# Kernel tuning notes

Hardware: AMD Instinct MI355X
Metric: run time of the kernel (lower is better)

The kernel has to match this reference:

```python
import jax, jax.numpy as jnp
import numpy as np

GRID_SIZE = 8
SPLINE_ORDER = 3
LAYERS = [256, 512, 512, 256]  # [input_dim] + hidden_dims
BATCH = 8192
BN_EPS = 1e-5


def make_grid(in_features):
    # efficient-kan/torchkan grid: uniform on [-1, 1] extended by spline_order on each side
    h = 2.0 / GRID_SIZE
    g = jnp.arange(-SPLINE_ORDER, GRID_SIZE + SPLINE_ORDER + 1, dtype=jnp.float32) * h - 1.0
    return jnp.broadcast_to(g, (in_features, g.shape[0]))  # (In, G + 2k + 1)


def b_splines(x, grid):
    # x: (B, In), grid: (In, G + 2k + 1) -> bases: (B, In, G + k)
    xg = x[:, :, None]
    bases = ((xg >= grid[:, :-1]) & (xg < grid[:, 1:])).astype(x.dtype)
    for k in range(1, SPLINE_ORDER + 1):
        left = (xg - grid[:, : -(k + 1)]) / (grid[:, k:-1] - grid[:, : -(k + 1)])
        right = (grid[:, k + 1 :] - xg) / (grid[:, k + 1 :] - grid[:, 1:-k])
        bases = left * bases[:, :, :-1] + right * bases[:, :, 1:]
    return bases


def kan_linear(x, grid, base_w, spline_w):
    # base path: GELU (exact, matching torch.nn.GELU) then linear
    base_out = jax.nn.gelu(x, approximate=False) @ base_w.T
    spline_out = jnp.einsum('bik,oik->bo', b_splines(x, grid), spline_w)
    return base_out + spline_out


def setup_inputs() -> dict:
    key = jax.random.key(0)
    ks = jax.random.split(key, 16)
    inp = {'x': jax.random.normal(ks[0], (BATCH, LAYERS[0]), dtype=jnp.float32)}
    n_bases = GRID_SIZE + SPLINE_ORDER
    for i, (fin, fout) in enumerate(zip(LAYERS[:-1], LAYERS[1:])):
        scale = 1.0 / np.sqrt(fin)
        inp[f'grid{i}'] = make_grid(fin)
        inp[f'base_w{i}'] = jax.random.normal(ks[1 + 3 * i], (fout, fin), dtype=jnp.float32) * scale
        inp[f'spline_w{i}'] = jax.random.normal(ks[2 + 3 * i], (fout, fin, n_bases), dtype=jnp.float32) * (0.1 * scale)
    d_out = LAYERS[-1]
    inp['bn_gamma'] = jnp.ones((d_out,), dtype=jnp.float32)
    inp['bn_beta'] = jnp.zeros((d_out,), dtype=jnp.float32)
    inp['bn_mean'] = jax.random.normal(ks[10], (d_out,), dtype=jnp.float32) * 0.1
    inp['bn_var'] = jax.random.uniform(ks[11], (d_out,), dtype=jnp.float32, minval=0.5, maxval=1.5)
    return inp


def reference(x, grid0, base_w0, spline_w0, grid1, base_w1, spline_w1, grid2, base_w2, spline_w2, bn_gamma, bn_beta, bn_mean, bn_var):
    h = kan_linear(x, grid0, base_w0, spline_w0)
    h = kan_linear(h, grid1, base_w1, spline_w1)
    h = kan_linear(h, grid2, base_w2, spline_w2)
    # BatchNorm1d in eval mode (running stats); Dropout is identity at inference
    return bn_gamma * (h - bn_mean) * jax.lax.rsqrt(bn_var + BN_EPS) + bn_beta
```

## Files before the change

kernel.cpp:

```cpp
#include <hip/hip_runtime.h>
#include <hip/hip_bf16.h>
#include <cstdint>


typedef unsigned short ushort_t;
typedef __bf16 bf16x8 __attribute__((ext_vector_type(8)));
typedef float f32x4 __attribute__((ext_vector_type(4)));

__device__ __forceinline__ ushort_t f2bf(float f) {
    __bf16 h = (__bf16)f;
    return __builtin_bit_cast(ushort_t, h);
}

__device__ __forceinline__ void gload_lds16(const void* g, void* lds) {
    __builtin_amdgcn_global_load_lds(
        (const __attribute__((address_space(1))) unsigned int*)(uintptr_t)g,
        (__attribute__((address_space(3))) unsigned int*)(unsigned int)(uintptr_t)lds,
        16, 0, 0);
}

__device__ __forceinline__ void expand12(float x, ushort_t* o) {
    float x3 = x * x * x;
    float y  = 0.7978845608028654f * (x + 0.044715f * x3);
    float e  = __expf(2.0f * y);
    float th = 1.0f - 2.0f / (e + 1.0f);
    o[0] = f2bf(0.5f * x * (1.0f + th));
    float xs = (x + 1.75f) * 4.0f;
#pragma unroll
    for (int j = 0; j < 11; ++j) {
        float t  = xs - (float)j;
        float a  = fabsf(t - 2.0f);
        float p1 = (3.0f * a - 6.0f) * a * a + 4.0f;
        float c  = 2.0f - a;
        float p2 = c * c * c;
        float v  = (a <= 1.0f) ? p1 : fmaxf(p2, 0.0f);
        o[1 + j] = f2bf(v * (1.0f / 6.0f));
    }
}

template <bool SUM>
__global__ __launch_bounds__(256) void expand_kernel(
    const float* __restrict__ X0, const float* __restrict__ X1,
    ushort_t* __restrict__ A, int total2)
{
    int idx = blockIdx.x * 256 + threadIdx.x;
    if (idx >= total2) return;
    float2 h = *(const float2*)(X0 + 2 * (size_t)idx);
    if (SUM) {
        float2 h2 = *(const float2*)(X1 + 2 * (size_t)idx);
        h.x += h2.x; h.y += h2.y;
    }
    union { ushort_t us[24]; uint4 v[3]; } pk;
    expand12(h.x, pk.us);
    expand12(h.y, pk.us + 12);
    uint4* dst = (uint4*)(A + (size_t)idx * 24);
    dst[0] = pk.v[0]; dst[1] = pk.v[1]; dst[2] = pk.v[2];
}

__global__ __launch_bounds__(256) void pack_w_kernel(
    const float* __restrict__ bw, const float* __restrict__ sw,
    ushort_t* __restrict__ W, int total)
{
    int idx = blockIdx.x * 256 + threadIdx.x;
    if (idx >= total) return;
    union { ushort_t us[12]; uint2 v[3]; } pk;
    pk.us[0] = f2bf(bw[idx]);
    const float* s = sw + (size_t)idx * 11;
#pragma unroll
    for (int k = 0; k < 11; ++k) pk.us[1 + k] = f2bf(s[k]);
    uint2* dst = (uint2*)(W + (size_t)idx * 12);
    dst[0] = pk.v[0]; dst[1] = pk.v[1]; dst[2] = pk.v[2];
}

__global__ __launch_bounds__(256, 2) void gemm_kernel(
    const ushort_t* __restrict__ A,
    const ushort_t* __restrict__ W,
    float* __restrict__ C,
    int M, int N, int K, int kcps)
{
    __shared__ __align__(16) ushort_t As[128 * 64];
    __shared__ __align__(16) ushort_t Bs[128 * 64];

    const int t   = threadIdx.x;
    const int l   = t & 63;
    const int w   = t >> 6;
    const int wm  = w >> 1;
    const int wn  = w & 1;
    const int l15 = l & 15;
    const int q   = l >> 4;
    const int blockM = blockIdx.x * 128;
    const int blockN = blockIdx.y * 128;
    const int kb0 = blockIdx.z * kcps, kb1 = kb0 + kcps;
    float* Cz = C + (size_t)blockIdx.z * M * N;

    f32x4 acc[4][4];
#pragma unroll
    for (int i = 0; i < 4; ++i)
#pragma unroll
        for (int j = 0; j < 4; ++j) acc[i][j] = (f32x4){0.f, 0.f, 0.f, 0.f};

    for (int kb = kb0; kb < kb1; ++kb) {
        const int k0 = kb << 6;
#pragma unroll
        for (int it = 0; it < 4; ++it) {
            int s   = it * 256 + t;
            int row = s >> 3, c = s & 7;
            int g   = c ^ (row & 7);
            gload_lds16(A + ((size_t)(blockM + row) * K + k0 + g * 8), &As[s * 8]);
        }
#pragma unroll
        for (int it = 0; it < 4; ++it) {
            int s   = it * 256 + t;
            int row = s >> 3, c = s & 7;
            int g   = c ^ (row & 7);
            gload_lds16(W + ((size_t)(blockN + row) * K + k0 + g * 8), &Bs[s * 8]);
        }
        __syncthreads();

#pragma unroll
        for (int ks = 0; ks < 2; ++ks) {
            const int kc = ks * 4 + q;
            bf16x8 af[4], bf[4];
#pragma unroll
            for (int mi = 0; mi < 4; ++mi) {
                int m  = wm * 64 + mi * 16 + l15;
                int cs = kc ^ (m & 7);
                af[mi] = *(const bf16x8*)&As[(size_t)(m * 8 + cs) * 8];
            }
#pragma unroll
            for (int ni = 0; ni < 4; ++ni) {
                int n  = wn * 64 + ni * 16 + l15;
                int cs = kc ^ (n & 7);
                bf[ni] = *(const bf16x8*)&Bs[(size_t)(n * 8 + cs) * 8];
            }
#pragma unroll
            for (int mi = 0; mi < 4; ++mi)
#pragma unroll
                for (int ni = 0; ni < 4; ++ni)
                    acc[mi][ni] = __builtin_amdgcn_mfma_f32_16x16x32_bf16(
                        af[mi], bf[ni], acc[mi][ni], 0, 0, 0);
        }
        __syncthreads();
    }

#pragma unroll
    for (int ni = 0; ni < 4; ++ni) {
        int n = blockN + wn * 64 + ni * 16 + l15;
#pragma unroll
        for (int mi = 0; mi < 4; ++mi) {
            int mb = blockM + wm * 64 + mi * 16 + q * 4;
#pragma unroll
            for (int r = 0; r < 4; ++r)
                Cz[(size_t)(mb + r) * N + n] = acc[mi][ni][r];
        }
    }
}

__global__ __launch_bounds__(256) void bn_reduce_kernel(
    const float4* __restrict__ Q0, const float4* __restrict__ Q1,
    const float4* __restrict__ Q2, const float4* __restrict__ Q3,
    const float* __restrict__ gamma, const float* __restrict__ beta,
    const float* __restrict__ mean,  const float* __restrict__ var,
    float4* __restrict__ out, int n4)
{
    int i = blockIdx.x * 256 + threadIdx.x;
    if (i >= n4) return;
    float4 a = Q0[i], b = Q1[i], c = Q2[i], d = Q3[i];
    int nb = (i * 4) & 255;
    float4 g  = *(const float4*)(gamma + nb);
    float4 be = *(const float4*)(beta + nb);
    float4 mn = *(const float4*)(mean + nb);
    float4 vr = *(const float4*)(var + nb);
    float4 o;
    o.x = g.x * rsqrtf(vr.x + 1e-5f) * (a.x + b.x + c.x + d.x - mn.x) + be.x;
    o.y = g.y * rsqrtf(vr.y + 1e-5f) * (a.y + b.y + c.y + d.y - mn.y) + be.y;
    o.z = g.z * rsqrtf(vr.z + 1e-5f) * (a.z + b.z + c.z + d.z - mn.z) + be.z;
    o.w = g.w * rsqrtf(vr.w + 1e-5f) * (a.w + b.w + c.w + d.w - mn.w) + be.w;
    out[i] = o;
}

extern "C" void kernel_launch(void* const* d_in, const int* in_sizes, int n_in,
                              void* d_out, int out_size, void* d_ws, size_t ws_size,
                              hipStream_t stream) {
    const float* x     = (const float*)d_in[0];
    const float* bw0   = (const float*)d_in[2];
    const float* sw0   = (const float*)d_in[3];
    const float* bw1   = (const float*)d_in[5];
    const float* sw1   = (const float*)d_in[6];
    const float* bw2   = (const float*)d_in[8];
    const float* sw2   = (const float*)d_in[9];
    const float* gamma = (const float*)d_in[10];
    const float* beta  = (const float*)d_in[11];
    const float* mean  = (const float*)d_in[12];
    const float* var   = (const float*)d_in[13];

    char* ws = (char*)d_ws;
    ushort_t* Abuf = (ushort_t*)(ws);
    ushort_t* W0   = (ushort_t*)(ws + 100663296);
    ushort_t* W1   = (ushort_t*)(ws + 103809024);
    ushort_t* W2   = (ushort_t*)(ws + 110100480);
    float*    P0   = (float*)(ws + 113246208);
    float*    P1   = (float*)(ws + 130023424);
    float*    Q0   = (float*)(ws + 113246208);
    float*    Q1   = (float*)(ws + 121634816);
    float*    Q2   = (float*)(ws + 130023424);
    float*    Q3   = (float*)(ws + 138412032);
    float*    out  = (float*)d_out;

    pack_w_kernel<<<(512 * 256 + 255) / 256, 256, 0, stream>>>(bw0, sw0, W0, 512 * 256);
    pack_w_kernel<<<(512 * 512 + 255) / 256, 256, 0, stream>>>(bw1, sw1, W1, 512 * 512);
    pack_w_kernel<<<(256 * 512 + 255) / 256, 256, 0, stream>>>(bw2, sw2, W2, 256 * 512);

    expand_kernel<false><<<4096, 256, 0, stream>>>(x, nullptr, Abuf, 8192 * 256 / 2);
    {
        dim3 g(64, 4, 2);
        gemm_kernel<<<g, 256, 0, stream>>>(Abuf, W0, P0, 8192, 512, 3072, 24);
    }
    expand_kernel<true><<<8192, 256, 0, stream>>>(P0, P1, Abuf, 8192 * 512 / 2);
    {
        dim3 g(64, 4, 2);
        gemm_kernel<<<g, 256, 0, stream>>>(Abuf, W1, P0, 8192, 512, 6144, 48);
    }
    expand_kernel<true><<<8192, 256, 0, stream>>>(P0, P1, Abuf, 8192 * 512 / 2);
    {
        dim3 g(64, 2, 4);
        gemm_kernel<<<g, 256, 0, stream>>>(Abuf, W2, Q0, 8192, 256, 6144, 24);
    }
    bn_reduce_kernel<<<2048, 256, 0, stream>>>(
        (const float4*)Q0, (const float4*)Q1, (const float4*)Q2, (const float4*)Q3,
        gamma, beta, mean, var, (float4*)out, 8192 * 256 / 4);
}
```

Baseline: 305.1 us.

## Rewrite GEMM as 128x256 tile with triple-buffered LDS prefetch pipeline

The GEMM now uses 512-thread blocks, each computing a 128x256 output tile with 8 waves (2x4). K-tiles are staged into three LDS slots held in dynamic shared memory, loading two tiles ahead. The loads are interleaved with four MFMA phases per tile, separated by barriers, raised scheduling priority (s_setprio) and explicit vmcnt and lgkmcnt waits. The aim is to hide global-to-LDS latency and improve operand reuse. The costs are 144 KB of LDS per block, which limits occupancy, many more barriers per tile, and a grid half as wide in N.

Measured after the change: 303.9 us. No clear change (-0.4%).

```diff
diff --git a/kernel.cpp b/kernel.cpp
--- a/kernel.cpp
+++ b/kernel.cpp
@@ -72,75 +72,172 @@
     dst[0] = pk.v[0]; dst[1] = pk.v[1]; dst[2] = pk.v[2];
 }
 
-__global__ __launch_bounds__(256, 2) void gemm_kernel(
+#define SLOT 24576
+#define ASZ  8192
+
+__global__ __launch_bounds__(512, 2) void gemm_kernel(
     const ushort_t* __restrict__ A,
     const ushort_t* __restrict__ W,
     float* __restrict__ C,
     int M, int N, int K, int kcps)
 {
-    __shared__ __align__(16) ushort_t As[128 * 64];
-    __shared__ __align__(16) ushort_t Bs[128 * 64];
+    extern __shared__ __align__(16) ushort_t lds[];
 
     const int t   = threadIdx.x;
     const int l   = t & 63;
     const int w   = t >> 6;
-    const int wm  = w >> 1;
-    const int wn  = w & 1;
+    const int wm  = w >> 2;
+    const int wn  = w & 3;
     const int l15 = l & 15;
     const int q   = l >> 4;
     const int blockM = blockIdx.x * 128;
-    const int blockN = blockIdx.y * 128;
-    const int kb0 = blockIdx.z * kcps, kb1 = kb0 + kcps;
+    const int blockN = blockIdx.y * 256;
+    const int kb0 = blockIdx.z * kcps;
+    const int nt  = kcps;
     float* Cz = C + (size_t)blockIdx.z * M * N;
 
-    f32x4 acc[4][4];
-#pragma unroll
-    for (int i = 0; i < 4; ++i)
-#pragma unroll
-        for (int j = 0; j < 4; ++j) acc[i][j] = (f32x4){0.f, 0.f, 0.f, 0.f};
-
-    for (int kb = kb0; kb < kb1; ++kb) {
-        const int k0 = kb << 6;
-#pragma unroll
-        for (int it = 0; it < 4; ++it) {
-            int s   = it * 256 + t;
+    const ushort_t* Ab = A + (size_t)blockM * K;
+    const ushort_t* Wb = W + (size_t)blockN * K;
+
+    auto stage_a = [&](int kb, ushort_t* dst) {
+#pragma unroll
+        for (int it = 0; it < 2; ++it) {
+            int s   = it * 512 + t;
             int row = s >> 3, c = s & 7;
             int g   = c ^ (row & 7);
-            gload_lds16(A + ((size_t)(blockM + row) * K + k0 + g * 8), &As[s * 8]);
-        }
-#pragma unroll
-        for (int it = 0; it < 4; ++it) {
-            int s   = it * 256 + t;
+            gload_lds16(Ab + ((size_t)row * K + (kb << 6) + g * 8), dst + s * 8);
+        }
+    };
+    auto stage_b = [&](int kb, ushort_t* dst, int half) {
+#pragma unroll
+        for (int it = 0; it < 2; ++it) {
+            int s   = (half * 2 + it) * 512 + t;
             int row = s >> 3, c = s & 7;
             int g   = c ^ (row & 7);
-            gload_lds16(W + ((size_t)(blockN + row) * K + k0 + g * 8), &Bs[s * 8]);
-        }
-        __syncthreads();
-
-#pragma unroll
-        for (int ks = 0; ks < 2; ++ks) {
-            const int kc = ks * 4 + q;
-            bf16x8 af[4], bf[4];
-#pragma unroll
-            for (int mi = 0; mi < 4; ++mi) {
-                int m  = wm * 64 + mi * 16 + l15;
-                int cs = kc ^ (m & 7);
-                af[mi] = *(const bf16x8*)&As[(size_t)(m * 8 + cs) * 8];
-            }
+            gload_lds16(Wb + ((size_t)row * K + (kb << 6) + g * 8), dst + s * 8);
+        }
+    };
+
+    f32x4 acc[4][4];
+#pragma unroll
+    for (int i = 0; i < 4; ++i)
+#pragma unroll
+        for (int j = 0; j < 4; ++j) acc[i][j] = (f32x4){0.f, 0.f, 0.f, 0.f};
+
+    stage_a(kb0, lds);            stage_b(kb0, lds + ASZ, 0);       stage_b(kb0, lds + ASZ, 1);
+    stage_a(kb0 + 1, lds + SLOT); stage_b(kb0 + 1, lds + SLOT + ASZ, 0);
+    stage_b(kb0 + 1, lds + SLOT + ASZ, 1);
+    asm volatile("s_waitcnt vmcnt(6)" ::: "memory");
+    __builtin_amdgcn_s_barrier();
+
+    int cur = 0;
+    for (int tt = 0; tt < nt; ++tt) {
+        ushort_t* Ac = lds + cur * SLOT;
+        ushort_t* Bc = Ac + ASZ;
+        int nx = cur + 2; if (nx >= 3) nx -= 3;
+        ushort_t* An = lds + nx * SLOT;
+        ushort_t* Bn = An + ASZ;
+        const bool pre = (tt + 2 < nt);
+        const int  kbp = kb0 + tt + 2;
+
+        bf16x8 af[2], bf[4];
+
+        if (pre) stage_a(kbp, An);
+        {
+            const int kc = q;
 #pragma unroll
             for (int ni = 0; ni < 4; ++ni) {
-                int n  = wn * 64 + ni * 16 + l15;
-                int cs = kc ^ (n & 7);
-                bf[ni] = *(const bf16x8*)&Bs[(size_t)(n * 8 + cs) * 8];
-            }
-#pragma unroll
-            for (int mi = 0; mi < 4; ++mi)
-#pragma unroll
-                for (int ni = 0; ni < 4; ++ni)
-                    acc[mi][ni] = __builtin_amdgcn_mfma_f32_16x16x32_bf16(
-                        af[mi], bf[ni], acc[mi][ni], 0, 0, 0);
-        }
-        __syncthreads();
+                int n = wn * 64 + ni * 16 + l15;
+                bf[ni] = *(const bf16x8*)&Bc[(n * 8 + (kc ^ (n & 7))) * 8];
+            }
+#pragma unroll
+            for (int mi = 0; mi < 2; ++mi) {
+                int m = wm * 64 + mi * 16 + l15;
+                af[mi] = *(const bf16x8*)&Ac[(m * 8 + (kc ^ (m & 7))) * 8];
+            }
+        }
+        __builtin_amdgcn_s_barrier();
+        asm volatile("s_waitcnt lgkmcnt(0)" ::: "memory");
+        __builtin_amdgcn_s_setprio(1);
+#pragma unroll
+        for (int mi = 0; mi < 2; ++mi)
+#pragma unroll
+            for (int ni = 0; ni < 4; ++ni)
+                acc[mi][ni] = __builtin_amdgcn_mfma_f32_16x16x32_bf16(
+                    af[mi], bf[ni], acc[mi][ni], 0, 0, 0);
+        __builtin_amdgcn_s_setprio(0);
+        __builtin_amdgcn_s_barrier();
+
+        if (pre) stage_b(kbp, Bn, 0);
+        {
+            const int kc = q;
+#pragma unroll
+            for (int mi = 0; mi < 2; ++mi) {
+                int m = wm * 64 + (mi + 2) * 16 + l15;
+                af[mi] = *(const bf16x8*)&Ac[(m * 8 + (kc ^ (m & 7))) * 8];
+            }
+        }
+        __builtin_amdgcn_s_barrier();
+        asm volatile("s_waitcnt lgkmcnt(0)" ::: "memory");
+        __builtin_amdgcn_s_setprio(1);
+#pragma unroll
+        for (int mi = 0; mi < 2; ++mi)
+#pragma unroll
+            for (int ni = 0; ni < 4; ++ni)
+                acc[mi + 2][ni] = __builtin_amdgcn_mfma_f32_16x16x32_bf16(
+                    af[mi], bf[ni], acc[mi + 2][ni], 0, 0, 0);
+        __builtin_amdgcn_s_setprio(0);
+        __builtin_amdgcn_s_barrier();
+
+        if (pre) stage_b(kbp, Bn, 1);
+        {
+            const int kc = 4 + q;
+#pragma unroll
+            for (int ni = 0; ni < 4; ++ni) {
+                int n = wn * 64 + ni * 16 + l15;
+                bf[ni] = *(const bf16x8*)&Bc[(n * 8 + (kc ^ (n & 7))) * 8];
+            }
+#pragma unroll
+            for (int mi = 0; mi < 2; ++mi) {
+                int m = wm * 64 + mi * 16 + l15;
+                af[mi] = *(const bf16x8*)&Ac[(m * 8 + (kc ^ (m & 7))) * 8];
+            }
+        }
+        __builtin_amdgcn_s_barrier();
+        asm volatile("s_waitcnt lgkmcnt(0)" ::: "memory");
+        __builtin_amdgcn_s_setprio(1);
+#pragma unroll
+        for (int mi = 0; mi < 2; ++mi)
+#pragma unroll
+            for (int ni = 0; ni < 4; ++ni)
+                acc[mi][ni] = __builtin_amdgcn_mfma_f32_16x16x32_bf16(
+                    af[mi], bf[ni], acc[mi][ni], 0, 0, 0);
+        __builtin_amdgcn_s_setprio(0);
+        __builtin_amdgcn_s_barrier();
+
+        {
+            const int kc = 4 + q;
+#pragma unroll
+            for (int mi = 0; mi < 2; ++mi) {
+                int m = wm * 64 + (mi + 2) * 16 + l15;
+                af[mi] = *(const bf16x8*)&Ac[(m * 8 + (kc ^ (m & 7))) * 8];
+            }
+        }
+        __builtin_amdgcn_s_barrier();
+        asm volatile("s_waitcnt lgkmcnt(0)" ::: "memory");
+        __builtin_amdgcn_s_setprio(1);
+#pragma unroll
+        for (int mi = 0; mi < 2; ++mi)
+#pragma unroll
+            for (int ni = 0; ni < 4; ++ni)
+                acc[mi + 2][ni] = __builtin_amdgcn_mfma_f32_16x16x32_bf16(
+                    af[mi], bf[ni], acc[mi + 2][ni], 0, 0, 0);
+        __builtin_amdgcn_s_setprio(0);
+        if (pre) asm volatile("s_waitcnt vmcnt(6)" ::: "memory");
+        else     asm volatile("s_waitcnt vmcnt(0)" ::: "memory");
+        __builtin_amdgcn_s_barrier();
+
+        cur = cur + 1; if (cur == 3) cur = 0;
     }
 
 #pragma unroll
@@ -207,24 +304,26 @@
     float*    Q3   = (float*)(ws + 138412032);
     float*    out  = (float*)d_out;
 
+    const size_t GEMM_LDS = 3 * SLOT * sizeof(ushort_t);
+
     pack_w_kernel<<<(512 * 256 + 255) / 256, 256, 0, stream>>>(bw0, sw0, W0, 512 * 256);
     pack_w_kernel<<<(512 * 512 + 255) / 256, 256, 0, stream>>>(bw1, sw1, W1, 512 * 512);
     pack_w_kernel<<<(256 * 512 + 255) / 256, 256, 0, stream>>>(bw2, sw2, W2, 256 * 512);
 
     expand_kernel<false><<<4096, 256, 0, stream>>>(x, nullptr, Abuf, 8192 * 256 / 2);
     {
-        dim3 g(64, 4, 2);
-        gemm_kernel<<<g, 256, 0, stream>>>(Abuf, W0, P0, 8192, 512, 3072, 24);
+        dim3 g(64, 2, 2);
+        gemm_kernel<<<g, 512, GEMM_LDS, stream>>>(Abuf, W0, P0, 8192, 512, 3072, 24);
     }
     expand_kernel<true><<<8192, 256, 0, stream>>>(P0, P1, Abuf, 8192 * 512 / 2);
     {
-        dim3 g(64, 4, 2);
-        gemm_kernel<<<g, 256, 0, stream>>>(Abuf, W1, P0, 8192, 512, 6144, 48);
+        dim3 g(64, 2, 2);
+        gemm_kernel<<<g, 512, GEMM_LDS, stream>>>(Abuf, W1, P0, 8192, 512, 6144, 48);
     }
     expand_kernel<true><<<8192, 256, 0, stream>>>(P0, P1, Abuf, 8192 * 512 / 2);
     {
-        dim3 g(64, 2, 4);
-        gemm_kernel<<<g, 256, 0, stream>>>(Abuf, W2, Q0, 8192, 256, 6144, 24);
+        dim3 g(64, 1, 4);
+        gemm_kernel<<<g, 512, GEMM_LDS, stream>>>(Abuf, W2, Q0, 8192, 256, 6144, 24);
     }
     bn_reduce_kernel<<<2048, 256, 0, stream>>>(
         (const float4*)Q0, (const float4*)Q1, (const float4*)Q2, (const float4*)Q3,
```
